# Performance work log

Hardware: AMD Instinct MI355X
Metric: run time of the kernel (lower is better)

Reference implementation:

```python
import jax, jax.numpy as jnp
import numpy as np

KY, KX = 3, 3  # kernel_size from init_kwargs


def setup_inputs() -> dict:
    key = jax.random.key(0)
    x = jax.random.normal(key, (8, 64, 256, 256), dtype=jnp.float32)
    return {"x": x}


def reference(x):
    # NMS: mask = x > max over 3x3 replicate-padded neighborhood EXCLUDING center.
    # Note: the torch conv kernel zeroes the center row, so the center output
    # channel is all zeros and the max implicitly includes 0 — we replicate that
    # by initializing the running max to zeros.
    ky, kx = KY, KX
    py, px = (ky - 1) // 2, (kx - 1) // 2
    H, W = x.shape[-2], x.shape[-1]
    xp = jnp.pad(x, ((0, 0), (0, 0), (py, py), (px, px)), mode='edge')  # replicate pad
    numel = ky * kx
    center = numel // 2
    max_non_center = jnp.zeros_like(x)  # zeroed-center channel participates in max
    for i in range(numel):  # fixed small kernel window, unrolled (8 shifts)
        if i == center:
            continue
        dy, dx = divmod(i, kx)
        max_non_center = jnp.maximum(max_non_center, xp[..., dy:dy + H, dx:dx + W])
    mask = x > max_non_center
    return x * mask.astype(x.dtype)
```

## Files before the change

kernel.cpp:

```cpp
#include <hip/hip_runtime.h>


#define NMS_H 256
#define NMS_W 256
#define ROWS 8

typedef float f4_t __attribute__((ext_vector_type(4)));

struct RowMax {
    float4 h;
    float4 lr;
};

__device__ __forceinline__ RowMax rowmax(const float4 v, const int tx) {
    float l = __shfl_up(v.w, 1, 64);
    float r = __shfl_down(v.x, 1, 64);
    if (tx == 0)  l = v.x;
    if (tx == 63) r = v.w;
    RowMax o;
    o.h.x = fmaxf(l,   fmaxf(v.x, v.y));
    o.h.y = fmaxf(v.x, fmaxf(v.y, v.z));
    o.h.z = fmaxf(v.y, fmaxf(v.z, v.w));
    o.h.w = fmaxf(v.z, fmaxf(v.w, r));
    o.lr.x = fmaxf(l,   v.y);
    o.lr.y = fmaxf(v.x, v.z);
    o.lr.z = fmaxf(v.y, v.w);
    o.lr.w = fmaxf(v.z, r);
    return o;
}

__global__ __launch_bounds__(256) void nms2d_kernel(const float* __restrict__ x,
                                                    float* __restrict__ out) {
    const int plane_idx = blockIdx.x >> 3;
    const int strip     = blockIdx.x & 7;
    const int tx        = threadIdx.x;
    const int col4      = tx * 4;
    const int r0        = strip * (ROWS * 4) + threadIdx.y * ROWS;

    const float* plane  = x   + (size_t)plane_idx * (NMS_H * NMS_W);
    float*       oplane = out + (size_t)plane_idx * (NMS_H * NMS_W);

    float4 v[ROWS + 2];
    #pragma unroll
    for (int i = 0; i < ROWS + 2; ++i) {
        const int r = min(max(r0 + i - 1, 0), NMS_H - 1);
        v[i] = *reinterpret_cast<const float4*>(plane + r * NMS_W + col4);
    }

    RowMax a = rowmax(v[0], tx);
    RowMax b = rowmax(v[1], tx);

    #pragma unroll
    for (int i = 0; i < ROWS; ++i) {
        RowMax c = rowmax(v[i + 2], tx);
        const float4 ctr = v[i + 1];
        float4 o;
        float m;
        m = fmaxf(0.0f, fmaxf(fmaxf(a.h.x, c.h.x), b.lr.x)); o.x = (ctr.x > m) ? ctr.x : 0.0f;
        m = fmaxf(0.0f, fmaxf(fmaxf(a.h.y, c.h.y), b.lr.y)); o.y = (ctr.y > m) ? ctr.y : 0.0f;
        m = fmaxf(0.0f, fmaxf(fmaxf(a.h.z, c.h.z), b.lr.z)); o.z = (ctr.z > m) ? ctr.z : 0.0f;
        m = fmaxf(0.0f, fmaxf(fmaxf(a.h.w, c.h.w), b.lr.w)); o.w = (ctr.w > m) ? ctr.w : 0.0f;

        f4_t ov = {o.x, o.y, o.z, o.w};
        __builtin_nontemporal_store(ov, reinterpret_cast<f4_t*>(oplane + (r0 + i) * NMS_W + col4));

        a = b; b = c;
    }
}

extern "C" void kernel_launch(void* const* d_in, const int* in_sizes, int n_in,
                              void* d_out, int out_size, void* d_ws, size_t ws_size,
                              hipStream_t stream) {
    const float* x = (const float*)d_in[0];
    float* out = (float*)d_out;

    dim3 block(64, 4);
    dim3 grid(512 * 8);
    nms2d_kernel<<<grid, block, 0, stream>>>(x, out);
}
```

Measured before the change: 230.2 us.

## Use persistent grid-stride waves processing 4-row groups

Replaces the fixed one-strip-per-wave mapping with a grid-stride loop over 4-row groups, launching half as many blocks. Each group loads 6 rows and computes all row maxima up front before emitting 4 output rows. This aims to cut launch/tail overhead and give more memory-level parallelism per wave, at the cost of a larger halo re-read ratio (6 loads per 4 rows instead of 10 per 8).

```diff
diff --git a/kernel.cpp b/kernel.cpp
--- a/kernel.cpp
+++ b/kernel.cpp
@@ -3,21 +3,23 @@
 
 #define NMS_H 256
 #define NMS_W 256
-#define ROWS 8
+#define PLANE (NMS_H * NMS_W)
+#define GROUPS_PER_PLANE (NMS_H / 4)
+#define NGROUPS (512 * GROUPS_PER_PLANE)
 
 typedef float f4_t __attribute__((ext_vector_type(4)));
 
-struct RowMax {
+struct HV {
     float4 h;
     float4 lr;
 };
 
-__device__ __forceinline__ RowMax rowmax(const float4 v, const int tx) {
+__device__ __forceinline__ HV rowmax(const float4 v, const int tx) {
     float l = __shfl_up(v.w, 1, 64);
     float r = __shfl_down(v.x, 1, 64);
     if (tx == 0)  l = v.x;
     if (tx == 63) r = v.w;
-    RowMax o;
+    HV o;
     o.h.x = fmaxf(l,   fmaxf(v.x, v.y));
     o.h.y = fmaxf(v.x, fmaxf(v.y, v.z));
     o.h.z = fmaxf(v.y, fmaxf(v.z, v.w));
@@ -31,40 +33,40 @@
 
 __global__ __launch_bounds__(256) void nms2d_kernel(const float* __restrict__ x,
                                                     float* __restrict__ out) {
-    const int plane_idx = blockIdx.x >> 3;
-    const int strip     = blockIdx.x & 7;
-    const int tx        = threadIdx.x;
-    const int col4      = tx * 4;
-    const int r0        = strip * (ROWS * 4) + threadIdx.y * ROWS;
+    const int tx    = threadIdx.x;
+    const int col4  = tx * 4;
+    const int wave  = blockIdx.x * blockDim.y + threadIdx.y;
+    const int nwave = gridDim.x * blockDim.y;
 
-    const float* plane  = x   + (size_t)plane_idx * (NMS_H * NMS_W);
-    float*       oplane = out + (size_t)plane_idx * (NMS_H * NMS_W);
+    for (int g = wave; g < NGROUPS; g += nwave) {
+        const int plane_idx = g >> 6;
+        const int r0        = (g & 63) * 4;
+        const float* pl = x   + (size_t)plane_idx * PLANE;
+        float*       op = out + (size_t)plane_idx * PLANE;
 
-    float4 v[ROWS + 2];
-    #pragma unroll
-    for (int i = 0; i < ROWS + 2; ++i) {
-        const int r = min(max(r0 + i - 1, 0), NMS_H - 1);
-        v[i] = *reinterpret_cast<const float4*>(plane + r * NMS_W + col4);
-    }
+        float4 v[6];
+        #pragma unroll
+        for (int i = 0; i < 6; ++i) {
+            const int r = min(max(r0 + i - 1, 0), NMS_H - 1);
+            v[i] = *reinterpret_cast<const float4*>(pl + r * NMS_W + col4);
+        }
 
-    RowMax a = rowmax(v[0], tx);
-    RowMax b = rowmax(v[1], tx);
+        HV m[6];
+        #pragma unroll
+        for (int i = 0; i < 6; ++i) m[i] = rowmax(v[i], tx);
 
-    #pragma unroll
-    for (int i = 0; i < ROWS; ++i) {
-        RowMax c = rowmax(v[i + 2], tx);
-        const float4 ctr = v[i + 1];
-        float4 o;
-        float m;
-        m = fmaxf(0.0f, fmaxf(fmaxf(a.h.x, c.h.x), b.lr.x)); o.x = (ctr.x > m) ? ctr.x : 0.0f;
-        m = fmaxf(0.0f, fmaxf(fmaxf(a.h.y, c.h.y), b.lr.y)); o.y = (ctr.y > m) ? ctr.y : 0.0f;
-        m = fmaxf(0.0f, fmaxf(fmaxf(a.h.z, c.h.z), b.lr.z)); o.z = (ctr.z > m) ? ctr.z : 0.0f;
-        m = fmaxf(0.0f, fmaxf(fmaxf(a.h.w, c.h.w), b.lr.w)); o.w = (ctr.w > m) ? ctr.w : 0.0f;
-
-        f4_t ov = {o.x, o.y, o.z, o.w};
-        __builtin_nontemporal_store(ov, reinterpret_cast<f4_t*>(oplane + (r0 + i) * NMS_W + col4));
-
-        a = b; b = c;
+        #pragma unroll
+        for (int i = 0; i < 4; ++i) {
+            const float4 ctr = v[i + 1];
+            const float4 ha = m[i].h, hb = m[i + 2].h, lc = m[i + 1].lr;
+            f4_t o;
+            float mm;
+            mm = fmaxf(0.0f, fmaxf(fmaxf(ha.x, hb.x), lc.x)); o.x = (ctr.x > mm) ? ctr.x : 0.0f;
+            mm = fmaxf(0.0f, fmaxf(fmaxf(ha.y, hb.y), lc.y)); o.y = (ctr.y > mm) ? ctr.y : 0.0f;
+            mm = fmaxf(0.0f, fmaxf(fmaxf(ha.z, hb.z), lc.z)); o.z = (ctr.z > mm) ? ctr.z : 0.0f;
+            mm = fmaxf(0.0f, fmaxf(fmaxf(ha.w, hb.w), lc.w)); o.w = (ctr.w > mm) ? ctr.w : 0.0f;
+            __builtin_nontemporal_store(o, reinterpret_cast<f4_t*>(op + (r0 + i) * NMS_W + col4));
+        }
     }
 }
 
@@ -75,6 +77,6 @@
     float* out = (float*)d_out;
 
     dim3 block(64, 4);
-    dim3 grid(512 * 8);
+    dim3 grid(2048);
     nms2d_kernel<<<grid, block, 0, stream>>>(x, out);
 }
```

Result: no change. 227.6 us (-1.1%).
